# Performance work log

Measured on AMD Instinct MI355X. Metric: run time of the kernel, lower is better.

## Reference

```python
import jax, jax.numpy as jnp
import numpy as np

N_NODES = 100000
N_EDGES = 1600000


def sage_conv(x, src, dst, W_self, W_neigh, b):
    # mean aggregation over incoming neighbors (DGL SAGEConv 'mean')
    msg = x[src]  # [E, d] gather
    agg = jax.ops.segment_sum(msg, dst, num_segments=N_NODES)
    deg = jax.ops.segment_sum(jnp.ones((src.shape[0],), x.dtype), dst, num_segments=N_NODES)
    h_neigh = agg / jnp.maximum(deg, 1.0)[:, None]
    return x @ W_self + h_neigh @ W_neigh + b


def setup_inputs() -> dict:
    key = jax.random.key(0)
    ks = jax.random.split(key, 9)
    x = jax.random.normal(ks[0], (N_NODES, 64), dtype=jnp.float32)
    src = jax.random.randint(ks[1], (N_EDGES,), 0, N_NODES)
    dst = jax.random.randint(ks[2], (N_EDGES,), 0, N_NODES)
    W_self1 = jax.random.normal(ks[3], (64, 32), dtype=jnp.float32) * 0.125
    W_neigh1 = jax.random.normal(ks[4], (64, 32), dtype=jnp.float32) * 0.125
    b1 = jnp.zeros((32,), jnp.float32)
    W_self2 = jax.random.normal(ks[5], (32, 16), dtype=jnp.float32) * 0.18
    W_neigh2 = jax.random.normal(ks[6], (32, 16), dtype=jnp.float32) * 0.18
    b2 = jnp.zeros((16,), jnp.float32)
    return {"x": x, "src": src, "dst": dst,
            "W_self1": W_self1, "W_neigh1": W_neigh1, "b1": b1,
            "W_self2": W_self2, "W_neigh2": W_neigh2, "b2": b2}


def reference(x, src, dst, W_self1, W_neigh1, b1, W_self2, W_neigh2, b2):
    h = sage_conv(x, src, dst, W_self1, W_neigh1, b1)   # [N, 32]
    h = sage_conv(h, src, dst, W_self2, W_neigh2, b2)   # [N, 16]
    return h
```

## Files before the change

### kernel.cpp

```cpp
#include <hip/hip_runtime.h>

#define NN 100000
#define NE 1600000
#define NPART 391
#define NC 391
#define CHUNK 4096
#define CAPB 4608
#define PROJ_NPB 64
#define PROJ_BLKS ((NN + PROJ_NPB - 1) / PROJ_NPB)

typedef float floatx2 __attribute__((ext_vector_type(2)));

__device__ __forceinline__ unsigned short f2bf(float f) {
    unsigned u = __float_as_uint(f);
    u = (u + 0x7FFFu + ((u >> 16) & 1u)) >> 16;
    return (unsigned short)u;
}
__device__ __forceinline__ float bflo(unsigned u) { return __uint_as_float(u << 16); }
__device__ __forceinline__ float bfhi(unsigned u) { return __uint_as_float(u & 0xFFFF0000u); }

__device__ __forceinline__ unsigned fp8enc(float f) {
    unsigned u = __float_as_uint(f);
    unsigned s = u >> 31;
    unsigned t = (u & 0x7FFFFFFFu) + 0x7FFFFu + ((u >> 20) & 1u);
    int e8 = (int)((t >> 23) & 255u) - 120;
    unsigned m = (t >> 20) & 7u;
    if (e8 <= 0) return s << 7;
    if (e8 > 15) { e8 = 15; m = 6; }
    return (s << 7) | ((unsigned)e8 << 3) | m;
}
__device__ __forceinline__ void acc8(float* a, uint2 v) {
    floatx2 p0 = __builtin_amdgcn_cvt_pk_f32_fp8(v.x, false);
    floatx2 p1 = __builtin_amdgcn_cvt_pk_f32_fp8(v.x, true);
    floatx2 p2 = __builtin_amdgcn_cvt_pk_f32_fp8(v.y, false);
    floatx2 p3 = __builtin_amdgcn_cvt_pk_f32_fp8(v.y, true);
    a[0] += p0[0]; a[1] += p0[1]; a[2] += p1[0]; a[3] += p1[1];
    a[4] += p2[0]; a[5] += p2[1]; a[6] += p3[0]; a[7] += p3[1];
}

struct BinSh {
    int hist[NPART];
    int scn[512];
    int cur[NPART];
    unsigned buf[CHUNK];
};
struct ProjSh {
    float Wcat[64 * 64];
    float bl[32];
    float4 Xl4[PROJ_NPB][17];
};

__global__ __launch_bounds__(512) void binproj_kernel(
    const int* __restrict__ src, const int* __restrict__ dst,
    unsigned* __restrict__ slots, int* __restrict__ cntCB, int* __restrict__ ofsCB,
    const float* __restrict__ X, const float* __restrict__ Wn1,
    const float* __restrict__ Ws1, const float* __restrict__ b1,
    unsigned char* __restrict__ P1, unsigned short* __restrict__ P1s)
{
    __shared__ union { BinSh b; ProjSh p; } sh;
    const int tid = threadIdx.x;
    if (blockIdx.x < NC) {
        const int c = blockIdx.x;
        for (int i = tid; i < NPART; i += 512) sh.b.hist[i] = 0;
        __syncthreads();
        const int e0 = c * CHUNK;
        const int e1 = (e0 + CHUNK < NE) ? e0 + CHUNK : NE;
        int      eb[8];
        unsigned pk[8];
#pragma unroll
        for (int u = 0; u < 8; ++u) {
            int e = e0 + tid + u * 512;
            if (e < e1) {
                int d = dst[e], s = src[e];
                eb[u] = d >> 8;
                pk[u] = ((unsigned)(d & 255) << 17) | (unsigned)s;
                atomicAdd(&sh.b.hist[eb[u]], 1);
            } else eb[u] = -1;
        }
        __syncthreads();
        int v = (tid < NPART) ? sh.b.hist[tid] : 0;
        sh.b.scn[tid] = v;
        __syncthreads();
        for (int d = 1; d < 512; d <<= 1) {
            int u = (tid >= d) ? sh.b.scn[tid - d] : 0;
            __syncthreads();
            sh.b.scn[tid] += u;
            __syncthreads();
        }
        const int excl = sh.b.scn[tid] - v;
        if (tid < NPART) {
            sh.b.cur[tid] = excl;
            cntCB[(size_t)c * NPART + tid] = v;
            ofsCB[(size_t)c * NPART + tid] = excl;
        }
        __syncthreads();
#pragma unroll
        for (int u = 0; u < 8; ++u) {
            if (eb[u] >= 0) {
                int pos = atomicAdd(&sh.b.cur[eb[u]], 1);
                sh.b.buf[pos] = pk[u];
            }
        }
        __syncthreads();
        const int m = e1 - e0;
        unsigned* op = slots + (size_t)c * CHUNK;
        for (int i = tid; i < m; i += 512) op[i] = sh.b.buf[i];
    } else {
        const int pb = blockIdx.x - NC;
        const int nbase = pb * PROJ_NPB;
        for (int i = tid; i < 64 * 64; i += 512) {
            int k = i >> 6, j = i & 63;
            sh.p.Wcat[i] = (j < 32) ? Wn1[k * 32 + j] : Ws1[k * 32 + (j - 32)];
        }
        if (tid < 32) sh.p.bl[tid] = b1[tid];
        for (int i = tid; i < PROJ_NPB * 16; i += 512) {
            int ln = i >> 4, k4 = i & 15;
            int n = nbase + ln;
            float4 xv = {0.f, 0.f, 0.f, 0.f};
            if (n < NN) xv = *reinterpret_cast<const float4*>(X + (size_t)n * 64 + k4 * 4);
            sh.p.Xl4[ln][k4] = xv;
        }
        __syncthreads();
        const int j4 = tid & 15;
        const int nl = tid >> 4;
        const int n0 = nbase + nl * 2;
        const int n1 = n0 + 1;
        const float4* W4 = reinterpret_cast<const float4*>(sh.p.Wcat);
        float4 a0 = {0.f,0.f,0.f,0.f}, a1 = {0.f,0.f,0.f,0.f};
        for (int k4 = 0; k4 < 16; ++k4) {
            const float4 x0 = sh.p.Xl4[nl * 2][k4];
            const float4 x1 = sh.p.Xl4[nl * 2 + 1][k4];
            const float* x0p = (const float*)&x0;
            const float* x1p = (const float*)&x1;
#pragma unroll
            for (int kk = 0; kk < 4; ++kk) {
                const float4 w = W4[(k4 * 4 + kk) * 16 + j4];
                const float v0 = x0p[kk], v1 = x1p[kk];
                a0.x += v0 * w.x; a0.y += v0 * w.y; a0.z += v0 * w.z; a0.w += v0 * w.w;
                a1.x += v1 * w.x; a1.y += v1 * w.y; a1.z += v1 * w.z; a1.w += v1 * w.w;
            }
        }
        if (j4 < 8) {
            unsigned pk0 = fp8enc(a0.x) | (fp8enc(a0.y) << 8) |
                           (fp8enc(a0.z) << 16) | (fp8enc(a0.w) << 24);
            unsigned pk1 = fp8enc(a1.x) | (fp8enc(a1.y) << 8) |
                           (fp8enc(a1.z) << 16) | (fp8enc(a1.w) << 24);
            if (n0 < NN) *reinterpret_cast<unsigned*>(P1 + (size_t)n0 * 32 + j4 * 4) = pk0;
            if (n1 < NN) *reinterpret_cast<unsigned*>(P1 + (size_t)n1 * 32 + j4 * 4) = pk1;
        } else {
            const int jb = (j4 - 8) * 4;
            const float4 bb = {sh.p.bl[jb], sh.p.bl[jb+1], sh.p.bl[jb+2], sh.p.bl[jb+3]};
            uint2 o0, o1;
            o0.x = (unsigned)f2bf(a0.x + bb.x) | ((unsigned)f2bf(a0.y + bb.y) << 16);
            o0.y = (unsigned)f2bf(a0.z + bb.z) | ((unsigned)f2bf(a0.w + bb.w) << 16);
            o1.x = (unsigned)f2bf(a1.x + bb.x) | ((unsigned)f2bf(a1.y + bb.y) << 16);
            o1.y = (unsigned)f2bf(a1.z + bb.z) | ((unsigned)f2bf(a1.w + bb.w) << 16);
            unsigned* P1su = (unsigned*)P1s;
            if (n0 < NN) *reinterpret_cast<uint2*>(P1su + (size_t)n0 * 16 + (j4 - 8) * 2) = o0;
            if (n1 < NN) *reinterpret_cast<uint2*>(P1su + (size_t)n1 * 16 + (j4 - 8) * 2) = o1;
        }
    }
}

__global__ __launch_bounds__(512) void csrfill_kernel(
    const unsigned* __restrict__ slots, const int* __restrict__ cntCB,
    const int* __restrict__ ofsCB, int* __restrict__ off, int* __restrict__ esrc)
{
    __shared__ unsigned ech[CAPB];
    __shared__ int s[512];
    __shared__ int myofs[NC], ccnt[NC];
    __shared__ int cntl[256], scn[256], curl[256];
    const int b = blockIdx.x, tid = threadIdx.x;

    int v = (tid < NC) ? cntCB[(size_t)tid * NPART + b] : 0;
    s[tid] = v;
    if (tid < NC) ccnt[tid] = v;
    __syncthreads();
    for (int d = 1; d < 512; d <<= 1) {
        int u = (tid >= d) ? s[tid - d] : 0;
        __syncthreads();
        s[tid] += u;
        __syncthreads();
    }
    if (tid < NC) myofs[tid] = s[tid] - v;
    __syncthreads();
    int total = s[NC - 1];
    if (total > CAPB) total = CAPB;

    if (tid < NC) {
        const int cnt = ccnt[tid];
        const int d0  = myofs[tid];
        const unsigned* sp = slots + (size_t)tid * CHUNK + ofsCB[(size_t)tid * NPART + b];
        for (int k = 0; k < cnt; ++k) {
            int p = d0 + k;
            if (p < CAPB) ech[p] = sp[k];
        }
    }
    if (tid < 256) cntl[tid] = 0;
    __syncthreads();

    for (int i = tid; i < total; i += 512) atomicAdd(&cntl[ech[i] >> 17], 1);
    __syncthreads();
    int nv = (tid < 256) ? cntl[tid] : 0;
    if (tid < 256) scn[tid] = nv;
    __syncthreads();
    for (int d = 1; d < 256; d <<= 1) {
        int u = (tid >= d && tid < 256) ? scn[tid - d] : 0;
        __syncthreads();
        if (tid < 256) scn[tid] += u;
        __syncthreads();
    }
    const int base  = b * CAPB;
    const int nbase = b << 8;
    const int nmax  = (NN - nbase < 256) ? (NN - nbase) : 256;
    if (tid < nmax) off[nbase + tid] = base + scn[tid];
    if (tid < 256)  curl[tid] = base + scn[tid] - nv;
    __syncthreads();
    for (int i = tid; i < total; i += 512) {
        unsigned ev = ech[i];
        int pos = atomicAdd(&curl[ev >> 17], 1);
        esrc[pos] = (int)(ev & 0x1FFFFu);
    }
}

__global__ __launch_bounds__(256) void aggproj1_kernel(
    const unsigned* __restrict__ P1, const int* __restrict__ esrc,
    const int* __restrict__ off, const unsigned* __restrict__ P1s,
    const float* __restrict__ Wn2, const float* __restrict__ Ws2,
    const float* __restrict__ b2,
    unsigned* __restrict__ P2, unsigned* __restrict__ S2)
{
    __shared__ float W2l[32 * 16];
    __shared__ float W3l[32 * 16];
    __shared__ float b2l[16];
    __shared__ float accL[32][33];
    __shared__ float Hl[32][33];
    const int tid = threadIdx.x;
    const int nbase = blockIdx.x * 32;
    for (int i = tid; i < 32 * 16; i += 256) W2l[i] = Wn2[i];
    for (int i = tid; i < 32 * 16; i += 256) W3l[i] = Ws2[i];
    if (tid < 16) b2l[tid] = b2[tid];
    const int ln  = tid >> 3;
    const int q   = tid & 7;
    const int sub = q >> 2;
    const int f4  = q & 3;
    const int n   = nbase + ln;
    float a[8] = {0,0,0,0,0,0,0,0};
    int e0 = 0, e1 = 0;
    if (n < NN) {
        e0 = (n & 255) ? off[n - 1] : (n >> 8) * CAPB;
        e1 = off[n];
        int e = e0 + sub;
        for (; e + 14 < e1; e += 16) {
            int sA[8];
#pragma unroll
            for (int u = 0; u < 8; ++u) sA[u] = esrc[e + 2 * u];
            uint2 vA[8];
#pragma unroll
            for (int u = 0; u < 8; ++u)
                vA[u] = *reinterpret_cast<const uint2*>(P1 + (size_t)sA[u] * 8 + f4 * 2);
#pragma unroll
            for (int u = 0; u < 8; ++u) acc8(a, vA[u]);
        }
        for (; e + 6 < e1; e += 8) {
            int s0 = esrc[e], s1 = esrc[e+2], s2 = esrc[e+4], s3 = esrc[e+6];
            const uint2 v0 = *reinterpret_cast<const uint2*>(P1 + (size_t)s0 * 8 + f4 * 2);
            const uint2 v1 = *reinterpret_cast<const uint2*>(P1 + (size_t)s1 * 8 + f4 * 2);
            const uint2 v2 = *reinterpret_cast<const uint2*>(P1 + (size_t)s2 * 8 + f4 * 2);
            const uint2 v3 = *reinterpret_cast<const uint2*>(P1 + (size_t)s3 * 8 + f4 * 2);
            acc8(a, v0); acc8(a, v1); acc8(a, v2); acc8(a, v3);
        }
        for (; e < e1; e += 2) {
            int s0 = esrc[e];
            const uint2 v0 = *reinterpret_cast<const uint2*>(P1 + (size_t)s0 * 8 + f4 * 2);
            acc8(a, v0);
        }
    }
#pragma unroll
    for (int i = 0; i < 8; ++i) a[i] += __shfl_xor(a[i], 4);
    if (sub == 0) {
#pragma unroll
        for (int i = 0; i < 8; ++i) accL[ln][f4 * 8 + i] = a[i];
    }
    __syncthreads();
    float d = (float)(e1 - e0);
    if (d < 1.f) d = 1.f;
    const float inv = 1.f / d;
    float r[4] = {0.f, 0.f, 0.f, 0.f};
    if (n < NN) {
        const uint2 sp = *reinterpret_cast<const uint2*>(P1s + (size_t)n * 16 + q * 2);
        r[0] = accL[ln][q * 4 + 0] * inv + bflo(sp.x);
        r[1] = accL[ln][q * 4 + 1] * inv + bfhi(sp.x);
        r[2] = accL[ln][q * 4 + 2] * inv + bflo(sp.y);
        r[3] = accL[ln][q * 4 + 3] * inv + bfhi(sp.y);
    }
#pragma unroll
    for (int i = 0; i < 4; ++i) Hl[ln][q * 4 + i] = r[i];
    __syncthreads();
    const int j2 = q * 2;
    float p2[2] = {0.f, 0.f}, s2[2] = {b2l[j2], b2l[j2 + 1]};
#pragma unroll
    for (int k = 0; k < 32; ++k) {
        float hv = Hl[ln][k];
        p2[0] += hv * W2l[k * 16 + j2];
        p2[1] += hv * W2l[k * 16 + j2 + 1];
        s2[0] += hv * W3l[k * 16 + j2];
        s2[1] += hv * W3l[k * 16 + j2 + 1];
    }
    if (n < NN) {
        P2[(size_t)n * 8 + q] = (unsigned)f2bf(p2[0]) | ((unsigned)f2bf(p2[1]) << 16);
        S2[(size_t)n * 8 + q] = (unsigned)f2bf(s2[0]) | ((unsigned)f2bf(s2[1]) << 16);
    }
}

__global__ __launch_bounds__(256) void aggproj2_kernel(
    const unsigned* __restrict__ P2, const int* __restrict__ esrc,
    const int* __restrict__ off, const unsigned* __restrict__ S2,
    float* __restrict__ out)
{
    __shared__ float accL[32][17];
    const int tid = threadIdx.x;
    const int nbase = blockIdx.x * 32;
    const int ln  = tid >> 3;
    const int q   = tid & 7;
    const int sub = q >> 2;
    const int f4  = q & 3;
    const int n   = nbase + ln;
    float a[4] = {0.f, 0.f, 0.f, 0.f};
    int e0 = 0, e1 = 0;
    if (n < NN) {
        e0 = (n & 255) ? off[n - 1] : (n >> 8) * CAPB;
        e1 = off[n];
        int e = e0 + sub;
        for (; e + 14 < e1; e += 16) {
            int sA[8];
#pragma unroll
            for (int u = 0; u < 8; ++u) sA[u] = esrc[e + 2 * u];
            uint2 vA[8];
#pragma unroll
            for (int u = 0; u < 8; ++u)
                vA[u] = *reinterpret_cast<const uint2*>(P2 + (size_t)sA[u] * 8 + f4 * 2);
#pragma unroll
            for (int u = 0; u < 8; ++u) {
                a[0] += bflo(vA[u].x); a[1] += bfhi(vA[u].x);
                a[2] += bflo(vA[u].y); a[3] += bfhi(vA[u].y);
            }
        }
        for (; e + 6 < e1; e += 8) {
            int s0 = esrc[e], s1 = esrc[e+2], s2 = esrc[e+4], s3 = esrc[e+6];
            const uint2 v0 = *reinterpret_cast<const uint2*>(P2 + (size_t)s0 * 8 + f4 * 2);
            const uint2 v1 = *reinterpret_cast<const uint2*>(P2 + (size_t)s1 * 8 + f4 * 2);
            const uint2 v2 = *reinterpret_cast<const uint2*>(P2 + (size_t)s2 * 8 + f4 * 2);
            const uint2 v3 = *reinterpret_cast<const uint2*>(P2 + (size_t)s3 * 8 + f4 * 2);
            a[0] += bflo(v0.x) + bflo(v1.x) + bflo(v2.x) + bflo(v3.x);
            a[1] += bfhi(v0.x) + bfhi(v1.x) + bfhi(v2.x) + bfhi(v3.x);
            a[2] += bflo(v0.y) + bflo(v1.y) + bflo(v2.y) + bflo(v3.y);
            a[3] += bfhi(v0.y) + bfhi(v1.y) + bfhi(v2.y) + bfhi(v3.y);
        }
        for (; e < e1; e += 2) {
            int s0 = esrc[e];
            const uint2 v0 = *reinterpret_cast<const uint2*>(P2 + (size_t)s0 * 8 + f4 * 2);
            a[0] += bflo(v0.x); a[1] += bfhi(v0.x);
            a[2] += bflo(v0.y); a[3] += bfhi(v0.y);
        }
    }
#pragma unroll
    for (int i = 0; i < 4; ++i) a[i] += __shfl_xor(a[i], 4);
    if (sub == 0) {
#pragma unroll
        for (int i = 0; i < 4; ++i) accL[ln][f4 * 4 + i] = a[i];
    }
    __syncthreads();
    if (n >= NN) return;
    float d = (float)(e1 - e0);
    if (d < 1.f) d = 1.f;
    const float inv = 1.f / d;
    const int j2 = q * 2;
    const unsigned sv = S2[(size_t)n * 8 + q];
    float2 o;
    o.x = accL[ln][j2]     * inv + bflo(sv);
    o.y = accL[ln][j2 + 1] * inv + bfhi(sv);
    *reinterpret_cast<float2*>(out + (size_t)n * 16 + j2) = o;
}

extern "C" void kernel_launch(void* const* d_in, const int* in_sizes, int n_in,
                              void* d_out, int out_size, void* d_ws, size_t ws_size,
                              hipStream_t stream)
{
    const float* x   = (const float*)d_in[0];
    const int*   src = (const int*)d_in[1];
    const int*   dst = (const int*)d_in[2];
    const float* Ws1 = (const float*)d_in[3];
    const float* Wn1 = (const float*)d_in[4];
    const float* b1  = (const float*)d_in[5];
    const float* Ws2 = (const float*)d_in[6];
    const float* Wn2 = (const float*)d_in[7];
    const float* b2  = (const float*)d_in[8];
    float* out = (float*)d_out;

    char* ws = (char*)d_ws;
    int*            off   = (int*)(ws);
    int*            cntCB = (int*)(ws + (512u << 10));
    int*            ofsCB = (int*)(ws + (1152u << 10));
    int*            esrc  = (int*)(ws + (2u << 20));
    unsigned char*  P1    = (unsigned char*)(ws + (10u << 20));
    unsigned short* P1s   = (unsigned short*)(ws + (14u << 20));
    unsigned*       P2    = (unsigned*)(ws + (24u << 20));
    unsigned*       S2    = (unsigned*)(ws + (28u << 20));
    unsigned*       slots = (unsigned*)(ws + (40u << 20));

    binproj_kernel<<<NC + PROJ_BLKS, 512, 0, stream>>>(
        src, dst, slots, cntCB, ofsCB, x, Wn1, Ws1, b1, P1, P1s);
    csrfill_kernel<<<NPART, 512, 0, stream>>>(slots, cntCB, ofsCB, off, esrc);
    aggproj1_kernel<<<(NN + 31) / 32, 256, 0, stream>>>(
        (const unsigned*)P1, esrc, off, (const unsigned*)P1s, Wn2, Ws2, b2, P2, S2);
    aggproj2_kernel<<<(NN + 31) / 32, 256, 0, stream>>>(
        P2, esrc, off, S2, out);
}
```

Before: 93.48 us.

## Hold projection weights in registers and double nodes per projection block

The first-layer projection branch now keeps each thread's weight column in registers instead of staging the concatenated weight matrix in shared memory. Each wavefront handles 16 nodes, with one output column per lane, and output bytes are packed through lane shuffles before storing. PROJ_NPB goes from 64 to 128, halving the number of projection blocks. The goal is fewer LDS weight reads and less per-block setup, at the cost of 64 extra VGPRs per thread, which may hurt occupancy, and narrower scattered stores.

After: 157.8 us. 1.69x slower.

```diff
diff --git a/kernel.cpp b/kernel.cpp
--- a/kernel.cpp
+++ b/kernel.cpp
@@ -6,7 +6,7 @@
 #define NC 391
 #define CHUNK 4096
 #define CAPB 4608
-#define PROJ_NPB 64
+#define PROJ_NPB 128
 #define PROJ_BLKS ((NN + PROJ_NPB - 1) / PROJ_NPB)
 
 typedef float floatx2 __attribute__((ext_vector_type(2)));
@@ -45,8 +45,6 @@
     unsigned buf[CHUNK];
 };
 struct ProjSh {
-    float Wcat[64 * 64];
-    float bl[32];
     float4 Xl4[PROJ_NPB][17];
 };
 
@@ -108,11 +106,24 @@
     } else {
         const int pb = blockIdx.x - NC;
         const int nbase = pb * PROJ_NPB;
-        for (int i = tid; i < 64 * 64; i += 512) {
-            int k = i >> 6, j = i & 63;
-            sh.p.Wcat[i] = (j < 32) ? Wn1[k * 32 + j] : Ws1[k * 32 + (j - 32)];
-        }
-        if (tid < 32) sh.p.bl[tid] = b1[tid];
+        const int j = tid & 63;
+        const int wv = tid >> 6;
+        float4 wreg[16];
+#pragma unroll
+        for (int k4 = 0; k4 < 16; ++k4) {
+            if (j < 32) {
+                wreg[k4].x = Wn1[(k4 * 4 + 0) * 32 + j];
+                wreg[k4].y = Wn1[(k4 * 4 + 1) * 32 + j];
+                wreg[k4].z = Wn1[(k4 * 4 + 2) * 32 + j];
+                wreg[k4].w = Wn1[(k4 * 4 + 3) * 32 + j];
+            } else {
+                wreg[k4].x = Ws1[(k4 * 4 + 0) * 32 + (j - 32)];
+                wreg[k4].y = Ws1[(k4 * 4 + 1) * 32 + (j - 32)];
+                wreg[k4].z = Ws1[(k4 * 4 + 2) * 32 + (j - 32)];
+                wreg[k4].w = Ws1[(k4 * 4 + 3) * 32 + (j - 32)];
+            }
+        }
+        const float blr = (j >= 32) ? b1[j - 32] : 0.f;
         for (int i = tid; i < PROJ_NPB * 16; i += 512) {
             int ln = i >> 4, k4 = i & 15;
             int n = nbase + ln;
@@ -121,43 +132,39 @@
             sh.p.Xl4[ln][k4] = xv;
         }
         __syncthreads();
-        const int j4 = tid & 15;
-        const int nl = tid >> 4;
-        const int n0 = nbase + nl * 2;
-        const int n1 = n0 + 1;
-        const float4* W4 = reinterpret_cast<const float4*>(sh.p.Wcat);
-        float4 a0 = {0.f,0.f,0.f,0.f}, a1 = {0.f,0.f,0.f,0.f};
-        for (int k4 = 0; k4 < 16; ++k4) {
-            const float4 x0 = sh.p.Xl4[nl * 2][k4];
-            const float4 x1 = sh.p.Xl4[nl * 2 + 1][k4];
-            const float* x0p = (const float*)&x0;
-            const float* x1p = (const float*)&x1;
-#pragma unroll
-            for (int kk = 0; kk < 4; ++kk) {
-                const float4 w = W4[(k4 * 4 + kk) * 16 + j4];
-                const float v0 = x0p[kk], v1 = x1p[kk];
-                a0.x += v0 * w.x; a0.y += v0 * w.y; a0.z += v0 * w.z; a0.w += v0 * w.w;
-                a1.x += v1 * w.x; a1.y += v1 * w.y; a1.z += v1 * w.z; a1.w += v1 * w.w;
+        unsigned* P1u  = (unsigned*)P1;
+        unsigned* P1su = (unsigned*)P1s;
+        const int lbase = wv * 16;
+        for (int g4 = 0; g4 < 4; ++g4) {
+            const int l0 = lbase + g4 * 4;
+            float acc[4] = {0.f, 0.f, 0.f, 0.f};
+#pragma unroll
+            for (int k4 = 0; k4 < 16; ++k4) {
+                const float4 w4 = wreg[k4];
+#pragma unroll
+                for (int gg = 0; gg < 4; ++gg) {
+                    const float4 xv = sh.p.Xl4[l0 + gg][k4];
+                    acc[gg] += xv.x * w4.x + xv.y * w4.y + xv.z * w4.z + xv.w * w4.w;
+                }
             }
-        }
-        if (j4 < 8) {
-            unsigned pk0 = fp8enc(a0.x) | (fp8enc(a0.y) << 8) |
-                           (fp8enc(a0.z) << 16) | (fp8enc(a0.w) << 24);
-            unsigned pk1 = fp8enc(a1.x) | (fp8enc(a1.y) << 8) |
-                           (fp8enc(a1.z) << 16) | (fp8enc(a1.w) << 24);
-            if (n0 < NN) *reinterpret_cast<unsigned*>(P1 + (size_t)n0 * 32 + j4 * 4) = pk0;
-            if (n1 < NN) *reinterpret_cast<unsigned*>(P1 + (size_t)n1 * 32 + j4 * 4) = pk1;
-        } else {
-            const int jb = (j4 - 8) * 4;
-            const float4 bb = {sh.p.bl[jb], sh.p.bl[jb+1], sh.p.bl[jb+2], sh.p.bl[jb+3]};
-            uint2 o0, o1;
-            o0.x = (unsigned)f2bf(a0.x + bb.x) | ((unsigned)f2bf(a0.y + bb.y) << 16);
-            o0.y = (unsigned)f2bf(a0.z + bb.z) | ((unsigned)f2bf(a0.w + bb.w) << 16);
-            o1.x = (unsigned)f2bf(a1.x + bb.x) | ((unsigned)f2bf(a1.y + bb.y) << 16);
-            o1.y = (unsigned)f2bf(a1.z + bb.z) | ((unsigned)f2bf(a1.w + bb.w) << 16);
-            unsigned* P1su = (unsigned*)P1s;
-            if (n0 < NN) *reinterpret_cast<uint2*>(P1su + (size_t)n0 * 16 + (j4 - 8) * 2) = o0;
-            if (n1 < NN) *reinterpret_cast<uint2*>(P1su + (size_t)n1 * 16 + (j4 - 8) * 2) = o1;
+#pragma unroll
+            for (int gg = 0; gg < 4; ++gg) {
+                const int n = nbase + l0 + gg;
+                if (j < 32) {
+                    unsigned b = fp8enc(acc[gg]);
+                    unsigned p = __shfl_xor(b, 1);
+                    unsigned t = (j & 1) ? (p | (b << 8)) : (b | (p << 8));
+                    unsigned qq = __shfl_xor(t, 2);
+                    unsigned w32 = (j & 2) ? (qq | (t << 16)) : (t | (qq << 16));
+                    if ((j & 3) == 0 && n < NN) P1u[(size_t)n * 8 + (j >> 2)] = w32;
+                } else {
+                    const int jj = j - 32;
+                    unsigned h = (unsigned)f2bf(acc[gg] + blr);
+                    unsigned p = __shfl_xor(h, 1);
+                    unsigned w32 = (jj & 1) ? (p | (h << 16)) : (h | (p << 16));
+                    if ((jj & 1) == 0 && n < NN) P1su[(size_t)n * 16 + (jj >> 1)] = w32;
+                }
+            }
         }
     }
 }
```
